# Optimization experiments

Measured on AMD Instinct MI355X. Metric: run time of the kernel, lower is better.

Reference implementation:

```python
import jax, jax.numpy as jnp
import numpy as np

HID, AA, ESM = 128, 21, 320
D1 = HID + AA + ESM          # 469
N_GRAPHS = 64
BN_EPS = 1e-5


def _lin_params(key, din, dout):
    k1, k2 = jax.random.split(key)
    s = 1.0 / np.sqrt(din)
    W = jax.random.uniform(k1, (din, dout), jnp.float32, -s, s)
    b = jax.random.uniform(k2, (dout,), jnp.float32, -s, s)
    return W, b


def setup_inputs() -> dict:
    key = jax.random.key(0)
    ks = jax.random.split(key, 16)
    N, E = 30000, 480000
    inp = {
        'prot_x': jax.random.normal(ks[0], (N, 6485), jnp.float32),
        'prot_edge_index': jax.random.randint(ks[1], (2, E), 0, N, jnp.int64),
        'prot_batch': jnp.sort(jax.random.randint(ks[2], (N,), 0, N_GRAPHS, jnp.int64)),
    }
    inp['fl1_W'], inp['fl1_b'] = _lin_params(ks[3], 6165 - 21, HID)
    inp['fl2_W'], inp['fl2_b'] = _lin_params(ks[4], AA, AA)
    inp['fl3_W'], inp['fl3_b'] = _lin_params(ks[5], ESM, ESM)
    inp['pdb1_W'], inp['pdb1_b'] = _lin_params(ks[6], D1, D1)
    inp['pdb2_W'], inp['pdb2_b'] = _lin_params(ks[7], D1, 2 * D1)
    inp['af1_W'], inp['af1_b'] = _lin_params(ks[8], D1, D1)
    inp['af2_W'], inp['af2_b'] = _lin_params(ks[9], D1, 2 * D1)
    inp['pdb3_W'], inp['pdb3_b'] = _lin_params(ks[10], 4 * D1, 4 * D1)
    inp['fc1_W'], inp['fc1_b'] = _lin_params(ks[11], 4 * D1, 1024)
    inp['bn_g'] = jnp.ones((1024,), jnp.float32)
    inp['bn_b'] = jnp.zeros((1024,), jnp.float32)
    inp['fc2_W'], inp['fc2_b'] = _lin_params(ks[12], 1024, 486)
    return inp


def _gcn_graph(edge_index, n):
    # add self-loops, symmetric normalization D^-1/2 (A+I) D^-1/2
    loops = jnp.arange(n, dtype=edge_index.dtype)
    src = jnp.concatenate([edge_index[0], loops])
    dst = jnp.concatenate([edge_index[1], loops])
    deg = jax.ops.segment_sum(jnp.ones_like(dst, jnp.float32), dst, n)
    dinv = jax.lax.rsqrt(jnp.maximum(deg, 1.0))  # deg >= 1 via self-loop
    norm = dinv[src] * dinv[dst]
    return src, dst, norm


def _gcn_conv(x, W, b, src, dst, norm, n):
    h = x @ W                                   # [N, Dout]
    msg = h[src] * norm[:, None]                # gather + scale
    return jax.ops.segment_sum(msg, dst, n) + b  # scatter-add


def reference(prot_x, prot_edge_index, prot_batch,
              fl1_W, fl1_b, fl2_W, fl2_b, fl3_W, fl3_b,
              pdb1_W, pdb1_b, pdb2_W, pdb2_b,
              af1_W, af1_b, af2_W, af2_b,
              pdb3_W, pdb3_b, fc1_W, fc1_b, bn_g, bn_b, fc2_W, fc2_b):
    n = prot_x.shape[0]
    relu = jax.nn.relu
    f1 = relu(prot_x[:, 21:6165] @ fl1_W + fl1_b)   # [N,128]
    f2 = relu(prot_x[:, :21] @ fl2_W + fl2_b)       # [N,21]
    f3 = relu(prot_x[:, 6165:] @ fl3_W + fl3_b)     # [N,320]
    feat = jnp.concatenate([f2, f1, f3], axis=1)    # [N,469]

    src, dst, norm = _gcn_graph(prot_edge_index, n)
    x = relu(_gcn_conv(feat, pdb1_W, pdb1_b, src, dst, norm, n))
    x = relu(_gcn_conv(x, pdb2_W, pdb2_b, src, dst, norm, n))
    y = relu(_gcn_conv(feat, af1_W, af1_b, src, dst, norm, n))
    y = relu(_gcn_conv(y, af2_W, af2_b, src, dst, norm, n))
    z = jnp.concatenate([x, y], axis=1)             # [N, 4*469]
    z = relu(_gcn_conv(z, pdb3_W, pdb3_b, src, dst, norm, n))

    # gap: global mean pool per graph
    cnt = jax.ops.segment_sum(jnp.ones((n,), jnp.float32), prot_batch, N_GRAPHS)
    z = jax.ops.segment_sum(z, prot_batch, N_GRAPHS) / jnp.maximum(cnt, 1.0)[:, None]

    z = z @ fc1_W + fc1_b                            # [G,1024]
    mu = jnp.mean(z, axis=0)
    var = jnp.mean((z - mu) ** 2, axis=0)            # biased, torch BN training math
    z = (z - mu) * jax.lax.rsqrt(var + BN_EPS) * bn_g + bn_b
    z = relu(z)                                      # dropout = identity (eval)
    z = z @ fc2_W + fc2_b
    return jax.nn.sigmoid(z)
```

## Files before the change

### kernel.cpp

```cpp
#include <hip/hip_runtime.h>
#include <hip/hip_bf16.h>
#include <stdint.h>

#define NG 64

typedef __attribute__((ext_vector_type(8))) short bf16x8;
typedef __attribute__((ext_vector_type(4))) float f32x4;

#define AS1 __attribute__((address_space(1)))
#define AS3 __attribute__((address_space(3)))

static __device__ __forceinline__ unsigned short f2b(float f) {
    unsigned u = __float_as_uint(f);
    return (unsigned short)((u + 0x7fffu + ((u >> 16) & 1u)) >> 16);
}
static __device__ __forceinline__ float b2f(unsigned short h) {
    return __uint_as_float(((unsigned)h) << 16);
}
static __device__ __forceinline__ void gl16(const void* g, void* l) {
    __builtin_amdgcn_global_load_lds(
        (const AS1 void*)(uintptr_t)g,
        (AS3 void*)(unsigned)(uintptr_t)l, 16, 0, 0);
}

__global__ void initcnt_k(int* cnt, int n) {
    int i = blockIdx.x * blockDim.x + threadIdx.x;
    if (i < n) cnt[i] = 0;
}
__global__ void count_k(const int* __restrict__ dst, int* cnt, int E) {
    int e = blockIdx.x * blockDim.x + threadIdx.x;
    if (e < E) atomicAdd(&cnt[dst[e]], 1);
}
__global__ void dinv_k(const int* __restrict__ cnt, float* dinv, int n) {
    int i = blockIdx.x * blockDim.x + threadIdx.x;
    if (i < n) dinv[i] = rsqrtf((float)(cnt[i] + 1));
}
__global__ void exscan_k(const int* __restrict__ cnt, int* rowptr, int n) {
    __shared__ int wsum[16];
    __shared__ int carry;
    int tid = threadIdx.x, lane = tid & 63, wid = tid >> 6;
    if (tid == 0) { carry = 0; rowptr[0] = 0; }
    __syncthreads();
    for (int base = 0; base < n; base += 1024) {
        int i = base + tid;
        int x = (i < n) ? cnt[i] : 0;
#pragma unroll
        for (int off = 1; off < 64; off <<= 1) {
            int t = __shfl_up(x, off);
            if (lane >= off) x += t;
        }
        if (lane == 63) wsum[wid] = x;
        __syncthreads();
        if (tid < 16) {
            int s = wsum[tid];
#pragma unroll
            for (int off = 1; off < 16; off <<= 1) {
                int t = __shfl_up(s, off);
                if (tid >= off) s += t;
            }
            wsum[tid] = s;
        }
        __syncthreads();
        int add = carry + (wid ? wsum[wid - 1] : 0);
        if (i < n) rowptr[i + 1] = x + add;
        __syncthreads();
        if (tid == 1023) carry = x + add;
        __syncthreads();
    }
}
__global__ void fillinit_k(const int* __restrict__ rowptr, int* fill, int n) {
    int i = blockIdx.x * blockDim.x + threadIdx.x;
    if (i < n) fill[i] = rowptr[i];
}
__global__ void fill_k(const int* __restrict__ src, const int* __restrict__ dst,
                       int* fill, int* csr, int E) {
    int e = blockIdx.x * blockDim.x + threadIdx.x;
    if (e < E) {
        int d = dst[e];
        int pos = atomicAdd(&fill[d], 1);
        csr[pos] = src[e];
    }
}

__global__ void wtconv_k(const float* __restrict__ W, int K, int Nout,
                         unsigned short* __restrict__ Wt, int Kpad, int Nrows) {
    __shared__ float t[32][33];
    int k0 = blockIdx.x * 32, n0 = blockIdx.y * 32;
    int cx = threadIdx.x & 31, ry = threadIdx.x >> 5;
#pragma unroll
    for (int p = 0; p < 4; ++p) {
        int k = k0 + ry + p * 8, nn = n0 + cx;
        t[ry + p * 8][cx] = (k < K && nn < Nout) ? W[(size_t)k * Nout + nn] : 0.0f;
    }
    __syncthreads();
#pragma unroll
    for (int p = 0; p < 4; ++p) {
        int nn = n0 + ry + p * 8, k = k0 + cx;
        if (nn < Nrows) Wt[(size_t)nn * Kpad + k] = f2b(t[cx][ry + p * 8]);
    }
}

__global__ void biascat_k(const float* __restrict__ b0, const float* __restrict__ b1,
                          float* __restrict__ out) {
    int i = threadIdx.x + blockIdx.x * blockDim.x;
    if (i >= 960) return;
    int seg = i >= 480, c = i - seg * 480;
    const float* b = seg ? b1 : b0;
    out[i] = (c < 469) ? b[c] : 0.0f;
}

__global__ void fl2_k(const float* __restrict__ x, int ldx,
                      const float* __restrict__ W, const float* __restrict__ b,
                      unsigned short* __restrict__ out, int ldo, int n) {
    __shared__ float Ws[441];
    __shared__ float Bs[21];
    int tid = threadIdx.x;
    for (int i = tid; i < 441; i += 256) Ws[i] = W[i];
    if (tid < 21) Bs[tid] = b[tid];
    __syncthreads();
    int row = blockIdx.x * 256 + tid;
    if (row >= n) return;
    float xv[21];
#pragma unroll
    for (int j = 0; j < 21; ++j) xv[j] = x[(size_t)row * ldx + j];
    for (int c = 0; c < 21; ++c) {
        float a = Bs[c];
#pragma unroll
        for (int j = 0; j < 21; ++j) a = fmaf(xv[j], Ws[j * 21 + c], a);
        out[(size_t)row * ldo + c] = f2b(fmaxf(a, 0.0f));
    }
}

template<bool A32>
__global__ __launch_bounds__(256) void mgemm_t(
    const void* __restrict__ Aptr, int lda, int Mreal,
    const unsigned short* __restrict__ Bt, int ldb,
    const float* __restrict__ bias,
    unsigned short* __restrict__ C, int ldc, int coff,
    int K, int Nout, int Nzero, int GX) {
    __shared__ unsigned short As[128 * 32];
    __shared__ unsigned short Bs[128 * 32];
    const int tid = threadIdx.x;
    const int w = tid >> 6, lane = tid & 63;

    const int nwg = gridDim.x;
    const int q = nwg >> 3, r = nwg & 7;
    const int xcd = blockIdx.x & 7, oidx = blockIdx.x >> 3;
    const int swz = (xcd < r ? xcd * (q + 1) : r * (q + 1) + (xcd - r) * q) + oidx;
    const int m0 = (swz / GX) * 128, n0 = (swz % GX) * 128;

    const int wr = w >> 1, wc = w & 1;

    f32x4 acc[4][4];
#pragma unroll
    for (int i = 0; i < 4; ++i)
#pragma unroll
        for (int j = 0; j < 4; ++j) acc[i][j] = (f32x4){0.f, 0.f, 0.f, 0.f};

    const int ko = (lane >> 4) * 8;
    const int rA = wr * 64 + (lane & 15);
    const int rB = wc * 64 + (lane & 15);

    for (int k0 = 0; k0 < K; k0 += 32) {
        if constexpr (A32) {
            const float* Af = (const float*)Aptr;
#pragma unroll
            for (int j = 0; j < 2; ++j) {
                int c = w * 2 + j;
                int id2 = c * 64 + lane;
                int row = id2 >> 2, cc = id2 & 3;
                int gm = m0 + row; if (gm > Mreal - 1) gm = Mreal - 1;
                const float* ap = Af + (size_t)gm * lda + k0 + cc * 8;
                float4 v0 = *(const float4*)ap;
                float4 v1 = *(const float4*)(ap + 4);
                unsigned short t[8] = {f2b(v0.x), f2b(v0.y), f2b(v0.z), f2b(v0.w),
                                       f2b(v1.x), f2b(v1.y), f2b(v1.z), f2b(v1.w)};
                *(bf16x8*)&As[row * 32 + cc * 8] = *(const bf16x8*)t;
            }
        } else {
            const unsigned short* Ab = (const unsigned short*)Aptr;
#pragma unroll
            for (int j = 0; j < 2; ++j) {
                int c = w * 2 + j;
                int id2 = c * 64 + lane;
                int row = id2 >> 2, cc = id2 & 3;
                gl16(Ab + (size_t)(m0 + row) * lda + k0 + cc * 8, &As[c * 512]);
            }
        }
#pragma unroll
        for (int j = 0; j < 2; ++j) {
            int c = w * 2 + j;
            int id2 = c * 64 + lane;
            int row = id2 >> 2, cc = id2 & 3;
            gl16(Bt + (size_t)(n0 + row) * ldb + k0 + cc * 8, &Bs[c * 512]);
        }
        __syncthreads();
        bf16x8 a[4], b[4];
#pragma unroll
        for (int i = 0; i < 4; ++i) a[i] = *(const bf16x8*)&As[(rA + i * 16) * 32 + ko];
#pragma unroll
        for (int j = 0; j < 4; ++j) b[j] = *(const bf16x8*)&Bs[(rB + j * 16) * 32 + ko];
#pragma unroll
        for (int i = 0; i < 4; ++i)
#pragma unroll
            for (int j = 0; j < 4; ++j)
                acc[i][j] = __builtin_amdgcn_mfma_f32_16x16x32_bf16(a[i], b[j], acc[i][j], 0, 0, 0);
        __syncthreads();
    }

    const int cn = lane & 15, r4 = (lane >> 4) * 4;
    for (int ni = 0; ni < 4; ++ni) {
        int col = n0 + wc * 64 + ni * 16 + cn;
        if (col >= Nzero) continue;
        bool real = col < Nout;
        float bb = real ? bias[col] : 0.0f;
#pragma unroll
        for (int mi = 0; mi < 4; ++mi) {
#pragma unroll
            for (int rr = 0; rr < 4; ++rr) {
                int row = m0 + wr * 64 + mi * 16 + r4 + rr;
                float x = real ? fmaxf(acc[mi][ni][rr] + bb, 0.0f) : 0.0f;
                C[(size_t)row * ldc + coff + col] = f2b(x);
            }
        }
    }
}

__global__ __launch_bounds__(256) void agg_wave_k(
    const unsigned short* __restrict__ in, unsigned short* __restrict__ out,
    const float* __restrict__ dinv, const int* __restrict__ rowptr,
    const int* __restrict__ csr, int D8, int ld, int n) {
    int lane = threadIdx.x & 63;
    int node = blockIdx.x * 4 + (threadIdx.x >> 6);
    if (node >= n) return;
    bool act = lane < D8;
    float di = dinv[node];
    float acc[8];
#pragma unroll
    for (int t = 0; t < 8; ++t) acc[t] = 0.0f;
    if (act) {
        bf16x8 v = *(const bf16x8*)(in + (size_t)node * ld + lane * 8);
#pragma unroll
        for (int t = 0; t < 8; ++t) acc[t] = di * b2f((unsigned short)v[t]);
    }
    int s = rowptr[node], e = rowptr[node + 1];
    for (int c = s; c < e; c += 64) {
        int m = e - c; if (m > 64) m = 64;
        int idx = (c + lane < e) ? csr[c + lane] : 0;
        float wl = dinv[idx];
        for (int j = 0; j < m; ++j) {
            int src = __shfl(idx, j);
            float wgt = __shfl(wl, j);
            if (act) {
                bf16x8 v = *(const bf16x8*)(in + (size_t)src * ld + lane * 8);
#pragma unroll
                for (int t = 0; t < 8; ++t) acc[t] = fmaf(wgt, b2f((unsigned short)v[t]), acc[t]);
            }
        }
    }
    if (act) {
        unsigned short o[8];
#pragma unroll
        for (int t = 0; t < 8; ++t) o[t] = f2b(di * acc[t]);
        *(bf16x8*)(out + (size_t)node * ld + lane * 8) = *(const bf16x8*)o;
    }
}

__global__ void agg_block_k(
    const unsigned short* __restrict__ in, unsigned short* __restrict__ out,
    const float* __restrict__ dinv, const int* __restrict__ rowptr,
    const int* __restrict__ csr, int D8, int ld, int n) {
    int i = blockIdx.x;
    int tid = threadIdx.x;
    __shared__ int s_src[64];
    __shared__ float s_w[64];
    bool act = tid < D8;
    float di = dinv[i];
    float acc[8];
#pragma unroll
    for (int t = 0; t < 8; ++t) acc[t] = 0.0f;
    if (act) {
        bf16x8 v = *(const bf16x8*)(in + (size_t)i * ld + tid * 8);
#pragma unroll
        for (int t = 0; t < 8; ++t) acc[t] = di * b2f((unsigned short)v[t]);
    }
    int s = rowptr[i], e = rowptr[i + 1];
    for (int c = s; c < e; c += 64) {
        int k = c + tid;
        if (tid < 64 && k < e) { int sn = csr[k]; s_src[tid] = sn; s_w[tid] = dinv[sn]; }
        __syncthreads();
        int m = e - c; if (m > 64) m = 64;
        for (int j = 0; j < m; ++j) {
            int sn = s_src[j];
            float wgt = s_w[j];
            if (act) {
                bf16x8 v = *(const bf16x8*)(in + (size_t)sn * ld + tid * 8);
#pragma unroll
                for (int t = 0; t < 8; ++t) acc[t] = fmaf(wgt, b2f((unsigned short)v[t]), acc[t]);
            }
        }
        __syncthreads();
    }
    if (act) {
        unsigned short o[8];
#pragma unroll
        for (int t = 0; t < 8; ++t) o[t] = f2b(di * acc[t]);
        *(bf16x8*)(out + (size_t)i * ld + tid * 8) = *(const bf16x8*)o;
    }
}

__global__ void pool_k(const unsigned short* __restrict__ in, int ld,
                       const int* __restrict__ batch,
                       float* __restrict__ out, int n, int D) {
    int g = blockIdx.y;
    int d = blockIdx.x * blockDim.x + threadIdx.x;
    if (d >= D) return;
    int lo = 0, hi = n;
    while (lo < hi) { int mid = (lo + hi) >> 1; if (batch[mid] < g) lo = mid + 1; else hi = mid; }
    int start = lo;
    lo = start; hi = n;
    while (lo < hi) { int mid = (lo + hi) >> 1; if (batch[mid] < g + 1) lo = mid + 1; else hi = mid; }
    int end = lo;
    float sum = 0.0f;
    for (int r = start; r < end; r++) sum += b2f(in[(size_t)r * ld + d]);
    out[(size_t)g * D + d] = sum / fmaxf((float)(end - start), 1.0f);
}

__global__ __launch_bounds__(256) void sgemm_part_k(
    const float* __restrict__ A, int lda,
    const float* __restrict__ W, int ldw,
    float* __restrict__ part, int K, int Nout, int ksplit) {
    const int n0 = blockIdx.x * 64;
    const int ks = blockIdx.y;
    const int kbeg = (int)(((long long)K * ks) / ksplit);
    const int kend = (int)(((long long)K * (ks + 1)) / ksplit);
    const int tx = threadIdx.x & 63, ty = threadIdx.x >> 6;
    __shared__ float As[64][65];
    float acc[16];
#pragma unroll
    for (int r = 0; r < 16; ++r) acc[r] = 0.0f;

    for (int kb = kbeg; kb < kend; kb += 64) {
        int kc = kend - kb; if (kc > 64) kc = 64;
        for (int i = threadIdx.x; i < 64 * 64; i += 256) {
            int r = i >> 6, c = i & 63;
            As[r][c] = (c < kc) ? A[(size_t)r * lda + kb + c] : 0.0f;
        }
        __syncthreads();
        if (n0 + tx < Nout) {
            for (int k = 0; k < kc; ++k) {
                float w = W[(size_t)(kb + k) * ldw + n0 + tx];
#pragma unroll
                for (int r = 0; r < 16; ++r)
                    acc[r] = fmaf(As[ty * 16 + r][k], w, acc[r]);
            }
        }
        __syncthreads();
    }
    if (n0 + tx < Nout) {
#pragma unroll
        for (int r = 0; r < 16; ++r)
            part[((size_t)ks * 64 + ty * 16 + r) * Nout + n0 + tx] = acc[r];
    }
}

__global__ void sgemm_reduce_k(const float* __restrict__ part, const float* __restrict__ bias,
                               float* __restrict__ C, int ldc, int Nout, int ksplit, int act) {
    int i = blockIdx.x * blockDim.x + threadIdx.x;
    if (i >= NG * Nout) return;
    int m = i / Nout, n = i - m * Nout;
    float v = bias[n];
    for (int s = 0; s < ksplit; ++s) v += part[((size_t)s * 64 + m) * Nout + n];
    if (act == 2) v = 1.0f / (1.0f + expf(-v));
    C[(size_t)m * ldc + n] = v;
}

__global__ void bn_k(const float* __restrict__ z, const float* __restrict__ g,
                     const float* __restrict__ b, float* __restrict__ out) {
    int c = blockIdx.x * blockDim.x + threadIdx.x;
    if (c >= 1024) return;
    float s = 0.0f, s2 = 0.0f;
    for (int r = 0; r < NG; r++) { float v = z[r * 1024 + c]; s += v; s2 += v * v; }
    float mu = s / (float)NG;
    float var = s2 / (float)NG - mu * mu;
    float sc = g[c] * rsqrtf(var + 1e-5f);
    float sh = b[c] - mu * sc;
    for (int r = 0; r < NG; r++)
        out[r * 1024 + c] = fmaxf(fmaf(z[r * 1024 + c], sc, sh), 0.0f);
}

extern "C" void kernel_launch(void* const* d_in, const int* in_sizes, int n_in,
                              void* d_out, int out_size, void* d_ws, size_t ws_size,
                              hipStream_t stream) {
    (void)n_in; (void)out_size; (void)ws_size;
    const float* prot_x = (const float*)d_in[0];
    const int*   eidx   = (const int*)d_in[1];
    const int*   batch  = (const int*)d_in[2];
    const float* fl1_W = (const float*)d_in[3],  *fl1_b = (const float*)d_in[4];
    const float* fl2_W = (const float*)d_in[5],  *fl2_b = (const float*)d_in[6];
    const float* fl3_W = (const float*)d_in[7],  *fl3_b = (const float*)d_in[8];
    const float* pdb1_W = (const float*)d_in[9],  *pdb1_b = (const float*)d_in[10];
    const float* pdb2_W = (const float*)d_in[11], *pdb2_b = (const float*)d_in[12];
    const float* af1_W  = (const float*)d_in[13], *af1_b  = (const float*)d_in[14];
    const float* af2_W  = (const float*)d_in[15], *af2_b  = (const float*)d_in[16];
    const float* pdb3_W = (const float*)d_in[17], *pdb3_b = (const float*)d_in[18];
    const float* fc1_W  = (const float*)d_in[19], *fc1_b  = (const float*)d_in[20];
    const float* bn_g   = (const float*)d_in[21], *bn_b   = (const float*)d_in[22];
    const float* fc2_W  = (const float*)d_in[23], *fc2_b  = (const float*)d_in[24];

    const int N = in_sizes[2];
    const int E = in_sizes[1] / 2;
    const int* e_src = eidx;
    const int* e_dst = eidx + E;
    const int Mpad = ((N + 127) / 128) * 128;
    const int MT = Mpad / 128;

    char* wp = (char*)d_ws;
    auto alloc = [&](size_t bytes) -> char* {
        char* r = wp; wp += (bytes + 255) & ~(size_t)255; return r;
    };
    unsigned short* feat = (unsigned short*)alloc((size_t)Mpad * 480 * 2);
    unsigned short* tmp1 = (unsigned short*)alloc((size_t)Mpad * 480 * 2);
    unsigned short* hxy  = (unsigned short*)alloc((size_t)Mpad * 960 * 2);
    unsigned short* tmp2 = (unsigned short*)alloc((size_t)Mpad * 960 * 2);
    unsigned short* zb   = (unsigned short*)alloc((size_t)Mpad * 1920 * 2);
    unsigned short* zagg = (unsigned short*)alloc((size_t)Mpad * 1920 * 2);
    unsigned short* zout = (unsigned short*)alloc((size_t)Mpad * 1888 * 2);
    unsigned short* wt_fl1  = (unsigned short*)alloc((size_t)128 * 6144 * 2);
    unsigned short* wt_fl3  = (unsigned short*)alloc((size_t)384 * 320 * 2);
    unsigned short* wt_c1   = (unsigned short*)alloc((size_t)1024 * 480 * 2);
    unsigned short* wt_pdb2 = (unsigned short*)alloc((size_t)1024 * 480 * 2);
    unsigned short* wt_af2  = (unsigned short*)alloc((size_t)1024 * 480 * 2);
    unsigned short* wt_pdb3 = (unsigned short*)alloc((size_t)1920 * 1920 * 2);
    float* f_bias1 = (float*)alloc(960 * 4);
    float* f_dinv = (float*)alloc((size_t)N * 4);
    float* f_pool = (float*)alloc((size_t)NG * 1876 * 4);
    float* f_fc1  = (float*)alloc((size_t)NG * 1024 * 4);
    float* f_bn   = (float*)alloc((size_t)NG * 1024 * 4);
    float* f_part = (float*)alloc((size_t)16 * 64 * 1024 * 4);
    int* i_cnt    = (int*)alloc((size_t)N * 4);
    int* i_rowptr = (int*)alloc((size_t)(N + 1) * 4);
    int* i_fill   = (int*)alloc((size_t)N * 4);
    int* i_csr    = (int*)alloc((size_t)E * 4);

    auto mg = [&](const unsigned short* A, int lda, const unsigned short* Wt, int ldb,
                  const float* bias, unsigned short* C, int ldc, int coff,
                  int K, int Nout, int Nzero) {
        int gx = (Nzero + 127) / 128;
        mgemm_t<false><<<gx * MT, 256, 0, stream>>>(
            A, lda, Mpad, Wt, ldb, bias, C, ldc, coff, K, Nout, Nzero, gx);
    };
    auto mgf = [&](const float* A, int lda, const unsigned short* Wt, int ldb,
                   const float* bias, unsigned short* C, int ldc, int coff,
                   int K, int Nout, int Nzero) {
        int gx = (Nzero + 127) / 128;
        mgemm_t<true><<<gx * MT, 256, 0, stream>>>(
            A, lda, N, Wt, ldb, bias, C, ldc, coff, K, Nout, Nzero, gx);
    };
    auto wt = [&](const float* W, int K, int Nout, unsigned short* Wt, int Kpad, int Nrows) {
        wtconv_k<<<dim3(Kpad / 32, Nrows / 32), 256, 0, stream>>>(W, K, Nout, Wt, Kpad, Nrows);
    };

    initcnt_k<<<(N + 255) / 256, 256, 0, stream>>>(i_cnt, N);
    count_k<<<(E + 255) / 256, 256, 0, stream>>>(e_dst, i_cnt, E);
    dinv_k<<<(N + 255) / 256, 256, 0, stream>>>(i_cnt, f_dinv, N);
    exscan_k<<<1, 1024, 0, stream>>>(i_cnt, i_rowptr, N);
    fillinit_k<<<(N + 255) / 256, 256, 0, stream>>>(i_rowptr, i_fill, N);
    fill_k<<<(E + 255) / 256, 256, 0, stream>>>(e_src, e_dst, i_fill, i_csr, E);

    wt(fl1_W, 6144, 128, wt_fl1, 6144, 128);
    wt(fl3_W, 320, 320, wt_fl3, 320, 384);
    wt(pdb1_W, 469, 469, wt_c1, 480, 480);
    wt(af1_W, 469, 469, wt_c1 + (size_t)480 * 480, 480, 544);
    wt(pdb2_W, 469, 938, wt_pdb2, 480, 1024);
    wt(af2_W, 469, 938, wt_af2, 480, 1024);
    wt(pdb3_W, 1876, 1876, wt_pdb3, 1920, 1920);
    biascat_k<<<4, 256, 0, stream>>>(pdb1_b, af1_b, f_bias1);

    fl2_k<<<(N + 255) / 256, 256, 0, stream>>>(prot_x, 6485, fl2_W, fl2_b, feat, 480, N);
    mgf(prot_x + 21,   6485, wt_fl1, 6144, fl1_b, feat, 480, 21,  6144, 128, 128);
    mgf(prot_x + 6165, 6485, wt_fl3, 320,  fl3_b, feat, 480, 149, 320,  320, 331);

    agg_wave_k<<<(N + 3) / 4, 256, 0, stream>>>(feat, tmp1, f_dinv, i_rowptr, i_csr, 60, 480, N);
    mg(tmp1, 480, wt_c1, 480, f_bias1, hxy, 960, 0, 480, 960, 960);
    agg_block_k<<<N, 128, 0, stream>>>(hxy, tmp2, f_dinv, i_rowptr, i_csr, 120, 960, N);
    mg(tmp2,       960, wt_pdb2, 480, pdb2_b, zb, 1920, 0,   480, 938, 938);
    mg(tmp2 + 480, 960, wt_af2,  480, af2_b,  zb, 1920, 938, 480, 938, 982);
    agg_block_k<<<N, 256, 0, stream>>>(zb, zagg, f_dinv, i_rowptr, i_csr, 240, 1920, N);
    mg(zagg, 1920, wt_pdb3, 1920, pdb3_b, zout, 1888, 0, 1920, 1876, 1876);

    pool_k<<<dim3((1876 + 255) / 256, NG), 256, 0, stream>>>(zout, 1888, batch, f_pool, N, 1876);
    sgemm_part_k<<<dim3(16, 16), 256, 0, stream>>>(f_pool, 1876, fc1_W, 1024, f_part, 1876, 1024, 16);
    sgemm_reduce_k<<<(NG * 1024 + 255) / 256, 256, 0, stream>>>(f_part, fc1_b, f_fc1, 1024, 1024, 16, 0);
    bn_k<<<4, 256, 0, stream>>>(f_fc1, bn_g, bn_b, f_bn);
    sgemm_part_k<<<dim3(8, 16), 256, 0, stream>>>(f_bn, 1024, fc2_W, 486, f_part, 1024, 486, 16);
    sgemm_reduce_k<<<(NG * 486 + 255) / 256, 256, 0, stream>>>(f_part, fc2_b, (float*)d_out, 486, 486, 16, 2);
}
```

Before: 1.742 ms.

## Split-K fl1 GEMM, parallel multi-block scan, vectorized pooling, aligned feature layout

Several changes land together. The single-block exclusive scan becomes a three-kernel multi-block scan. The fl1 GEMM, which has only 128 output columns, now uses split-K over three partitions plus a reduce kernel to fill more CUs. The feature layout is reordered so fl1 and fl3 land at aligned offsets and fl2 moves to the tail, with the conv1 weights row-remapped to match. Pooling now reads 8 bf16 values per thread. In exchange there is extra partial-sum traffic and more kernel launches. The pdb3 output pad columns are now zero-filled so the vectorized pooling can read them.

Measured after the change: 1.673 ms. 1.04x faster.

```diff
diff --git a/kernel.cpp b/kernel.cpp
--- a/kernel.cpp
+++ b/kernel.cpp
@@ -35,37 +35,50 @@
     int i = blockIdx.x * blockDim.x + threadIdx.x;
     if (i < n) dinv[i] = rsqrtf((float)(cnt[i] + 1));
 }
-__global__ void exscan_k(const int* __restrict__ cnt, int* rowptr, int n) {
+__global__ void scan1_k(const int* __restrict__ cnt, int* __restrict__ scan,
+                        int* __restrict__ bsum, int n) {
     __shared__ int wsum[16];
-    __shared__ int carry;
     int tid = threadIdx.x, lane = tid & 63, wid = tid >> 6;
-    if (tid == 0) { carry = 0; rowptr[0] = 0; }
+    int i = blockIdx.x * 1024 + tid;
+    int x = (i < n) ? cnt[i] : 0;
+#pragma unroll
+    for (int off = 1; off < 64; off <<= 1) {
+        int t = __shfl_up(x, off);
+        if (lane >= off) x += t;
+    }
+    if (lane == 63) wsum[wid] = x;
     __syncthreads();
-    for (int base = 0; base < n; base += 1024) {
-        int i = base + tid;
-        int x = (i < n) ? cnt[i] : 0;
-#pragma unroll
-        for (int off = 1; off < 64; off <<= 1) {
-            int t = __shfl_up(x, off);
-            if (lane >= off) x += t;
-        }
-        if (lane == 63) wsum[wid] = x;
-        __syncthreads();
-        if (tid < 16) {
-            int s = wsum[tid];
-#pragma unroll
-            for (int off = 1; off < 16; off <<= 1) {
-                int t = __shfl_up(s, off);
-                if (tid >= off) s += t;
-            }
-            wsum[tid] = s;
-        }
-        __syncthreads();
-        int add = carry + (wid ? wsum[wid - 1] : 0);
-        if (i < n) rowptr[i + 1] = x + add;
-        __syncthreads();
-        if (tid == 1023) carry = x + add;
-        __syncthreads();
+    if (tid < 16) {
+        int s = wsum[tid];
+#pragma unroll
+        for (int off = 1; off < 16; off <<= 1) {
+            int t = __shfl_up(s, off);
+            if (tid >= off) s += t;
+        }
+        wsum[tid] = s;
+    }
+    __syncthreads();
+    int add = wid ? wsum[wid - 1] : 0;
+    if (i < n) scan[i] = x + add;
+    if (tid == 1023) bsum[blockIdx.x] = x + add;
+}
+__global__ void scan2_k(int* bsum, int nb) {
+    int tid = threadIdx.x;
+    int x = (tid < nb) ? bsum[tid] : 0;
+#pragma unroll
+    for (int off = 1; off < 64; off <<= 1) {
+        int t = __shfl_up(x, off);
+        if (tid >= off) x += t;
+    }
+    if (tid < nb) bsum[tid] = x;
+}
+__global__ void scan3_k(const int* __restrict__ scan, const int* __restrict__ bsum,
+                        int* __restrict__ rowptr, int n) {
+    int i = blockIdx.x * blockDim.x + threadIdx.x;
+    if (i == 0) rowptr[0] = 0;
+    if (i < n) {
+        int b = i >> 10;
+        rowptr[i + 1] = scan[i] + (b ? bsum[b - 1] : 0);
     }
 }
 __global__ void fillinit_k(const int* __restrict__ rowptr, int* fill, int n) {
@@ -83,14 +96,22 @@
 }
 
 __global__ void wtconv_k(const float* __restrict__ W, int K, int Nout,
-                         unsigned short* __restrict__ Wt, int Kpad, int Nrows) {
+                         unsigned short* __restrict__ Wt, int Kpad, int Nrows, int remap) {
     __shared__ float t[32][33];
     int k0 = blockIdx.x * 32, n0 = blockIdx.y * 32;
     int cx = threadIdx.x & 31, ry = threadIdx.x >> 5;
 #pragma unroll
     for (int p = 0; p < 4; ++p) {
         int k = k0 + ry + p * 8, nn = n0 + cx;
-        t[ry + p * 8][cx] = (k < K && nn < Nout) ? W[(size_t)k * Nout + nn] : 0.0f;
+        int ko = k;
+        bool kvalid;
+        if (remap) {
+            ko = (k < 448) ? k + 21 : k - 448;
+            kvalid = (k < 469);
+        } else {
+            kvalid = (k < K);
+        }
+        t[ry + p * 8][cx] = (kvalid && nn < Nout) ? W[(size_t)ko * Nout + nn] : 0.0f;
     }
     __syncthreads();
 #pragma unroll
@@ -123,11 +144,15 @@
     float xv[21];
 #pragma unroll
     for (int j = 0; j < 21; ++j) xv[j] = x[(size_t)row * ldx + j];
-    for (int c = 0; c < 21; ++c) {
-        float a = Bs[c];
-#pragma unroll
-        for (int j = 0; j < 21; ++j) a = fmaf(xv[j], Ws[j * 21 + c], a);
-        out[(size_t)row * ldo + c] = f2b(fmaxf(a, 0.0f));
+    for (int c = 0; c < 32; ++c) {
+        float v = 0.0f;
+        if (c < 21) {
+            float a = Bs[c];
+#pragma unroll
+            for (int j = 0; j < 21; ++j) a = fmaf(xv[j], Ws[j * 21 + c], a);
+            v = fmaxf(a, 0.0f);
+        }
+        out[(size_t)row * ldo + 448 + c] = f2b(v);
     }
 }
 
@@ -226,6 +251,93 @@
     }
 }
 
+__global__ __launch_bounds__(256) void fl1part_k(
+    const float* __restrict__ A, int lda, int Mreal,
+    const unsigned short* __restrict__ Bt, int ldb,
+    float* __restrict__ part, int MT, int Mpad) {
+    __shared__ unsigned short As[128 * 32];
+    __shared__ unsigned short Bs[128 * 32];
+    const int tid = threadIdx.x;
+    const int w = tid >> 6, lane = tid & 63;
+    const int mt = blockIdx.x % MT, ks = blockIdx.x / MT;
+    const int m0 = mt * 128;
+    const int kbeg = ks * 2048, kend = kbeg + 2048;
+    const int wr = w >> 1, wc = w & 1;
+
+    f32x4 acc[4][4];
+#pragma unroll
+    for (int i = 0; i < 4; ++i)
+#pragma unroll
+        for (int j = 0; j < 4; ++j) acc[i][j] = (f32x4){0.f, 0.f, 0.f, 0.f};
+
+    const int ko = (lane >> 4) * 8;
+    const int rA = wr * 64 + (lane & 15);
+    const int rB = wc * 64 + (lane & 15);
+
+    for (int k0 = kbeg; k0 < kend; k0 += 32) {
+#pragma unroll
+        for (int j = 0; j < 2; ++j) {
+            int c = w * 2 + j;
+            int id2 = c * 64 + lane;
+            int row = id2 >> 2, cc = id2 & 3;
+            int gm = m0 + row; if (gm > Mreal - 1) gm = Mreal - 1;
+            const float* ap = A + (size_t)gm * lda + k0 + cc * 8;
+            float4 v0 = *(const float4*)ap;
+            float4 v1 = *(const float4*)(ap + 4);
+            unsigned short t[8] = {f2b(v0.x), f2b(v0.y), f2b(v0.z), f2b(v0.w),
+                                   f2b(v1.x), f2b(v1.y), f2b(v1.z), f2b(v1.w)};
+            *(bf16x8*)&As[row * 32 + cc * 8] = *(const bf16x8*)t;
+            gl16(Bt + (size_t)row * ldb + k0 + cc * 8, &Bs[c * 512]);
+        }
+        __syncthreads();
+        bf16x8 a[4], b[4];
+#pragma unroll
+        for (int i = 0; i < 4; ++i) a[i] = *(const bf16x8*)&As[(rA + i * 16) * 32 + ko];
+#pragma unroll
+        for (int j = 0; j < 4; ++j) b[j] = *(const bf16x8*)&Bs[(rB + j * 16) * 32 + ko];
+#pragma unroll
+        for (int i = 0; i < 4; ++i)
+#pragma unroll
+            for (int j = 0; j < 4; ++j)
+                acc[i][j] = __builtin_amdgcn_mfma_f32_16x16x32_bf16(a[i], b[j], acc[i][j], 0, 0, 0);
+        __syncthreads();
+    }
+
+    float* pb = part + (size_t)ks * Mpad * 128;
+    const int cn = lane & 15, r4 = (lane >> 4) * 4;
+#pragma unroll
+    for (int ni = 0; ni < 4; ++ni) {
+        int col = wc * 64 + ni * 16 + cn;
+#pragma unroll
+        for (int mi = 0; mi < 4; ++mi) {
+#pragma unroll
+            for (int rr = 0; rr < 4; ++rr) {
+                int row = m0 + wr * 64 + mi * 16 + r4 + rr;
+                pb[(size_t)row * 128 + col] = acc[mi][ni][rr];
+            }
+        }
+    }
+}
+
+__global__ void fl1red_k(const float* __restrict__ part, const float* __restrict__ bias,
+                         unsigned short* __restrict__ feat, int Mpad) {
+    int i = blockIdx.x * blockDim.x + threadIdx.x;
+    if (i >= Mpad * 32) return;
+    int row = i >> 5, c = (i & 31) * 4;
+    size_t base = (size_t)row * 128 + c;
+    size_t stride = (size_t)Mpad * 128;
+    float4 p0 = *(const float4*)(part + base);
+    float4 p1 = *(const float4*)(part + stride + base);
+    float4 p2 = *(const float4*)(part + 2 * stride + base);
+    float4 bb = *(const float4*)(bias + c);
+    ushort4 o;
+    o.x = f2b(fmaxf(p0.x + p1.x + p2.x + bb.x, 0.0f));
+    o.y = f2b(fmaxf(p0.y + p1.y + p2.y + bb.y, 0.0f));
+    o.z = f2b(fmaxf(p0.z + p1.z + p2.z + bb.z, 0.0f));
+    o.w = f2b(fmaxf(p0.w + p1.w + p2.w + bb.w, 0.0f));
+    *(ushort4*)(feat + (size_t)row * 480 + c) = o;
+}
+
 __global__ __launch_bounds__(256) void agg_wave_k(
     const unsigned short* __restrict__ in, unsigned short* __restrict__ out,
     const float* __restrict__ dinv, const int* __restrict__ rowptr,
@@ -313,17 +425,28 @@
                        const int* __restrict__ batch,
                        float* __restrict__ out, int n, int D) {
     int g = blockIdx.y;
-    int d = blockIdx.x * blockDim.x + threadIdx.x;
-    if (d >= D) return;
+    int d8 = blockIdx.x * blockDim.x + threadIdx.x;
+    if (d8 * 8 >= ld) return;
     int lo = 0, hi = n;
     while (lo < hi) { int mid = (lo + hi) >> 1; if (batch[mid] < g) lo = mid + 1; else hi = mid; }
     int start = lo;
     lo = start; hi = n;
     while (lo < hi) { int mid = (lo + hi) >> 1; if (batch[mid] < g + 1) lo = mid + 1; else hi = mid; }
     int end = lo;
-    float sum = 0.0f;
-    for (int r = start; r < end; r++) sum += b2f(in[(size_t)r * ld + d]);
-    out[(size_t)g * D + d] = sum / fmaxf((float)(end - start), 1.0f);
+    float s[8];
+#pragma unroll
+    for (int j = 0; j < 8; ++j) s[j] = 0.0f;
+    for (int r = start; r < end; r++) {
+        bf16x8 v = *(const bf16x8*)(in + (size_t)r * ld + d8 * 8);
+#pragma unroll
+        for (int j = 0; j < 8; ++j) s[j] += b2f((unsigned short)v[j]);
+    }
+    float inv = 1.0f / fmaxf((float)(end - start), 1.0f);
+#pragma unroll
+    for (int j = 0; j < 8; ++j) {
+        int d = d8 * 8 + j;
+        if (d < D) out[(size_t)g * D + d] = s[j] * inv;
+    }
 }
 
 __global__ __launch_bounds__(256) void sgemm_part_k(
@@ -414,6 +537,7 @@
     const int* e_dst = eidx + E;
     const int Mpad = ((N + 127) / 128) * 128;
     const int MT = Mpad / 128;
+    const int NB = (N + 1023) / 1024;
 
     char* wp = (char*)d_ws;
     auto alloc = [&](size_t bytes) -> char* {
@@ -438,7 +562,10 @@
     float* f_fc1  = (float*)alloc((size_t)NG * 1024 * 4);
     float* f_bn   = (float*)alloc((size_t)NG * 1024 * 4);
     float* f_part = (float*)alloc((size_t)16 * 64 * 1024 * 4);
+    float* f_flp  = (float*)alloc((size_t)3 * Mpad * 128 * 4);
     int* i_cnt    = (int*)alloc((size_t)N * 4);
+    int* i_scan   = (int*)alloc((size_t)N * 4);
+    int* i_bsum   = (int*)alloc(64 * 4);
     int* i_rowptr = (int*)alloc((size_t)(N + 1) * 4);
     int* i_fill   = (int*)alloc((size_t)N * 4);
     int* i_csr    = (int*)alloc((size_t)E * 4);
@@ -457,29 +584,32 @@
         mgemm_t<true><<<gx * MT, 256, 0, stream>>>(
             A, lda, N, Wt, ldb, bias, C, ldc, coff, K, Nout, Nzero, gx);
     };
-    auto wt = [&](const float* W, int K, int Nout, unsigned short* Wt, int Kpad, int Nrows) {
-        wtconv_k<<<dim3(Kpad / 32, Nrows / 32), 256, 0, stream>>>(W, K, Nout, Wt, Kpad, Nrows);
+    auto wt = [&](const float* W, int K, int Nout, unsigned short* Wt, int Kpad, int Nrows, int remap) {
+        wtconv_k<<<dim3(Kpad / 32, Nrows / 32), 256, 0, stream>>>(W, K, Nout, Wt, Kpad, Nrows, remap);
     };
 
     initcnt_k<<<(N + 255) / 256, 256, 0, stream>>>(i_cnt, N);
     count_k<<<(E + 255) / 256, 256, 0, stream>>>(e_dst, i_cnt, E);
     dinv_k<<<(N + 255) / 256, 256, 0, stream>>>(i_cnt, f_dinv, N);
-    exscan_k<<<1, 1024, 0, stream>>>(i_cnt, i_rowptr, N);
+    scan1_k<<<NB, 1024, 0, stream>>>(i_cnt, i_scan, i_bsum, N);
+    scan2_k<<<1, 64, 0, stream>>>(i_bsum, NB);
+    scan3_k<<<(N + 255) / 256, 256, 0, stream>>>(i_scan, i_bsum, i_rowptr, N);
     fillinit_k<<<(N + 255) / 256, 256, 0, stream>>>(i_rowptr, i_fill, N);
     fill_k<<<(E + 255) / 256, 256, 0, stream>>>(e_src, e_dst, i_fill, i_csr, E);
 
-    wt(fl1_W, 6144, 128, wt_fl1, 6144, 128);
-    wt(fl3_W, 320, 320, wt_fl3, 320, 384);
-    wt(pdb1_W, 469, 469, wt_c1, 480, 480);
-    wt(af1_W, 469, 469, wt_c1 + (size_t)480 * 480, 480, 544);
-    wt(pdb2_W, 469, 938, wt_pdb2, 480, 1024);
-    wt(af2_W, 469, 938, wt_af2, 480, 1024);
-    wt(pdb3_W, 1876, 1876, wt_pdb3, 1920, 1920);
+    wt(fl1_W, 6144, 128, wt_fl1, 6144, 128, 0);
+    wt(fl3_W, 320, 320, wt_fl3, 320, 384, 0);
+    wt(pdb1_W, 469, 469, wt_c1, 480, 480, 1);
+    wt(af1_W, 469, 469, wt_c1 + (size_t)480 * 480, 480, 544, 1);
+    wt(pdb2_W, 469, 938, wt_pdb2, 480, 1024, 0);
+    wt(af2_W, 469, 938, wt_af2, 480, 1024, 0);
+    wt(pdb3_W, 1876, 1876, wt_pdb3, 1920, 1920, 0);
     biascat_k<<<4, 256, 0, stream>>>(pdb1_b, af1_b, f_bias1);
 
     fl2_k<<<(N + 255) / 256, 256, 0, stream>>>(prot_x, 6485, fl2_W, fl2_b, feat, 480, N);
-    mgf(prot_x + 21,   6485, wt_fl1, 6144, fl1_b, feat, 480, 21,  6144, 128, 128);
-    mgf(prot_x + 6165, 6485, wt_fl3, 320,  fl3_b, feat, 480, 149, 320,  320, 331);
+    fl1part_k<<<MT * 3, 256, 0, stream>>>(prot_x + 21, 6485, N, wt_fl1, 6144, f_flp, MT, Mpad);
+    fl1red_k<<<(Mpad * 32 + 255) / 256, 256, 0, stream>>>(f_flp, fl1_b, feat, Mpad);
+    mgf(prot_x + 6165, 6485, wt_fl3, 320, fl3_b, feat, 480, 128, 320, 320, 320);
 
     agg_wave_k<<<(N + 3) / 4, 256, 0, stream>>>(feat, tmp1, f_dinv, i_rowptr, i_csr, 60, 480, N);
     mg(tmp1, 480, wt_c1, 480, f_bias1, hxy, 960, 0, 480, 960, 960);
@@ -487,9 +617,9 @@
     mg(tmp2,       960, wt_pdb2, 480, pdb2_b, zb, 1920, 0,   480, 938, 938);
     mg(tmp2 + 480, 960, wt_af2,  480, af2_b,  zb, 1920, 938, 480, 938, 982);
     agg_block_k<<<N, 256, 0, stream>>>(zb, zagg, f_dinv, i_rowptr, i_csr, 240, 1920, N);
-    mg(zagg, 1920, wt_pdb3, 1920, pdb3_b, zout, 1888, 0, 1920, 1876, 1876);
-
-    pool_k<<<dim3((1876 + 255) / 256, NG), 256, 0, stream>>>(zout, 1888, batch, f_pool, N, 1876);
+    mg(zagg, 1920, wt_pdb3, 1920, pdb3_b, zout, 1888, 0, 1920, 1876, 1888);
+
+    pool_k<<<dim3(2, NG), 128, 0, stream>>>(zout, 1888, batch, f_pool, N, 1876);
     sgemm_part_k<<<dim3(16, 16), 256, 0, stream>>>(f_pool, 1876, fc1_W, 1024, f_part, 1876, 1024, 16);
     sgemm_reduce_k<<<(NG * 1024 + 255) / 256, 256, 0, stream>>>(f_part, fc1_b, f_fc1, 1024, 1024, 16, 0);
     bn_k<<<4, 256, 0, stream>>>(f_fc1, bn_g, bn_b, f_bn);
```
